# Kernel tuning notes

Measured on AMD Instinct MI355X. Metric: run time of the kernel, lower is better.

## Reference

```python
import jax, jax.numpy as jnp
import numpy as np

N_EMB = 512
N_HEADS = 8
HEAD_SIZE = N_EMB // N_HEADS  # 64
B, T = 4, 2048
EPS = 1e-5


def layernorm(x, g, b):
    mu = jnp.mean(x, axis=-1, keepdims=True)
    var = jnp.var(x, axis=-1, keepdims=True)
    return (x - mu) * jax.lax.rsqrt(var + EPS) * g + b


def setup_inputs() -> dict:
    key = jax.random.key(0)
    ks = jax.random.split(key, 8)
    s = 1.0 / np.sqrt(N_EMB)
    x = jax.random.normal(ks[0], (B, T, N_EMB), dtype=jnp.float32)
    # per-head q/k/v weights stacked: [H, n_emb, head_size]
    wq = jax.random.uniform(ks[1], (N_HEADS, N_EMB, HEAD_SIZE), minval=-s, maxval=s, dtype=jnp.float32)
    wk = jax.random.uniform(ks[2], (N_HEADS, N_EMB, HEAD_SIZE), minval=-s, maxval=s, dtype=jnp.float32)
    wv = jax.random.uniform(ks[3], (N_HEADS, N_EMB, HEAD_SIZE), minval=-s, maxval=s, dtype=jnp.float32)
    w_ff = jax.random.uniform(ks[4], (N_EMB, N_EMB), minval=-s, maxval=s, dtype=jnp.float32)
    b_ff = jax.random.uniform(ks[5], (N_EMB,), minval=-s, maxval=s, dtype=jnp.float32)
    ln1_g = jnp.ones((N_EMB,), jnp.float32)
    ln1_b = jnp.zeros((N_EMB,), jnp.float32)
    ln2_g = jnp.ones((N_EMB,), jnp.float32)
    ln2_b = jnp.zeros((N_EMB,), jnp.float32)
    return {"x": x, "wq": wq, "wk": wk, "wv": wv, "w_ff": w_ff, "b_ff": b_ff,
            "ln1_g": ln1_g, "ln1_b": ln1_b, "ln2_g": ln2_g, "ln2_b": ln2_b}


def reference(x, wq, wk, wv, w_ff, b_ff, ln1_g, ln1_b, ln2_g, ln2_b):
    # --- self-attention branch (dropout=0 -> identity) ---
    h = layernorm(x, ln1_g, ln1_b)                       # [B,T,C]
    q = jnp.einsum('btc,hcd->bhtd', h, wq)               # [B,H,T,d]
    k = jnp.einsum('btc,hcd->bhtd', h, wk)
    v = jnp.einsum('btc,hcd->bhtd', h, wv)
    scale = HEAD_SIZE ** -0.5
    wei = jnp.einsum('bhtd,bhsd->bhts', q, k) * scale    # [B,H,T,T]
    Tt = x.shape[1]
    causal = jnp.tril(jnp.ones((Tt, Tt), dtype=bool))
    wei = jnp.where(causal, wei, -jnp.inf)
    wei = jax.nn.softmax(wei, axis=-1)
    attn = jnp.einsum('bhts,bhsd->bhtd', wei, v)         # [B,H,T,d]
    # concat heads along last dim (head order preserved)
    Bn, H, Tn, d = attn.shape
    sa = jnp.transpose(attn, (0, 2, 1, 3)).reshape(Bn, Tn, H * d)
    x = x + sa
    # --- feed-forward branch: Linear + ReLU (dropout=0) ---
    h2 = layernorm(x, ln2_g, ln2_b)
    ff = jax.nn.relu(h2 @ w_ff + b_ff)
    return x + ff
```

## Files before the change

### kernel.cpp

```cpp
#include <hip/hip_runtime.h>

#define Bsz  4
#define Tseq 2048
#define Cdim 512
#define Hn   8
#define Dh   64
#define BT   8192
#define NQKV 1536
#define NEG_BIG (-1e30f)

typedef __attribute__((ext_vector_type(8))) short bf16x8;
typedef __attribute__((ext_vector_type(4))) short bf16x4;
typedef __attribute__((ext_vector_type(4))) float f32x4;

__device__ __forceinline__ float b2f(short s) {
    unsigned u = ((unsigned)(unsigned short)s) << 16;
    float f; __builtin_memcpy(&f, &u, 4); return f;
}
__device__ __forceinline__ short f2b(float f) {
    unsigned u; __builtin_memcpy(&u, &f, 4);
    u = (u + 0x7fffu + ((u >> 16) & 1u)) >> 16;
    return (short)u;
}
__device__ __forceinline__ void g2l16(const short* g, short* l) {
    __builtin_amdgcn_global_load_lds(
        (const __attribute__((address_space(1))) unsigned int*)(uintptr_t)g,
        (__attribute__((address_space(3))) unsigned int*)l, 16, 0, 0);
}

__global__ __launch_bounds__(256) void k_prep(const float* __restrict__ wq, const float* __restrict__ wk,
                                              const float* __restrict__ wv, const float* __restrict__ wff,
                                              short* __restrict__ wqkvt, short* __restrict__ wfft,
                                              const float* __restrict__ x, const float* __restrict__ g,
                                              const float* __restrict__ b, short* __restrict__ out) {
    const int blk = blockIdx.x, tid = threadIdx.x;
    if (blk < 256) {
        __shared__ float ldsT[64 * 65];
        if (blk < 192) {
            int hm = blk >> 3, ct = blk & 7;
            int proj = hm >> 3, h = hm & 7;
            const float* w = (proj == 0) ? wq : (proj == 1 ? wk : wv);
#pragma unroll
            for (int i = 0; i < 16; i++) {
                int flat = i * 256 + tid, cc = flat >> 6, dd = flat & 63;
                ldsT[dd * 65 + cc] = w[(h * 512 + ct * 64 + cc) * 64 + dd];
            }
            __syncthreads();
#pragma unroll
            for (int i = 0; i < 16; i++) {
                int flat = i * 256 + tid, dd = flat >> 6, cc = flat & 63;
                int n = proj * 512 + h * 64 + dd;
                wqkvt[n * 512 + ct * 64 + cc] = f2b(ldsT[dd * 65 + cc]);
            }
        } else {
            int b2 = blk - 192, rt = b2 >> 3, nt8 = b2 & 7;
#pragma unroll
            for (int i = 0; i < 16; i++) {
                int flat = i * 256 + tid, cc = flat >> 6, nn = flat & 63;
                ldsT[nn * 65 + cc] = wff[(rt * 64 + cc) * 512 + nt8 * 64 + nn];
            }
            __syncthreads();
#pragma unroll
            for (int i = 0; i < 16; i++) {
                int flat = i * 256 + tid, nn = flat >> 6, cc = flat & 63;
                wfft[(nt8 * 64 + nn) * 512 + rt * 64 + cc] = f2b(ldsT[nn * 65 + cc]);
            }
        }
    } else {
        int row  = (blk - 256) * 4 + (tid >> 6);
        int lane = tid & 63;
        const f32x4 a0 = *(const f32x4*)(x + row * Cdim + lane * 8);
        const f32x4 a1 = *(const f32x4*)(x + row * Cdim + lane * 8 + 4);
        float v[8] = {a0[0], a0[1], a0[2], a0[3], a1[0], a1[1], a1[2], a1[3]};
        float s = 0.f, sq = 0.f;
#pragma unroll
        for (int i = 0; i < 8; i++) { s += v[i]; sq += v[i] * v[i]; }
#pragma unroll
        for (int off = 1; off < 64; off <<= 1) { s += __shfl_xor(s, off); sq += __shfl_xor(sq, off); }
        float mean = s * (1.f / 512.f);
        float var  = sq * (1.f / 512.f) - mean * mean;
        float rstd = rsqrtf(var + 1e-5f);
        const f32x4 g0 = *(const f32x4*)(g + lane * 8);
        const f32x4 g1 = *(const f32x4*)(g + lane * 8 + 4);
        const f32x4 b0 = *(const f32x4*)(b + lane * 8);
        const f32x4 b1 = *(const f32x4*)(b + lane * 8 + 4);
        float gg[8] = {g0[0], g0[1], g0[2], g0[3], g1[0], g1[1], g1[2], g1[3]};
        float bb[8] = {b0[0], b0[1], b0[2], b0[3], b1[0], b1[1], b1[2], b1[3]};
        bf16x8 o;
#pragma unroll
        for (int i = 0; i < 8; i++) o[i] = f2b((v[i] - mean) * rstd * gg[i] + bb[i]);
        *(bf16x8*)(out + row * Cdim + lane * 8) = o;
    }
}

__global__ __launch_bounds__(256) void k_ln(const float* __restrict__ x, const float* __restrict__ g,
                                            const float* __restrict__ b, short* __restrict__ out) {
    int row  = blockIdx.x * 4 + (threadIdx.x >> 6);
    int lane = threadIdx.x & 63;
    const f32x4 a0 = *(const f32x4*)(x + row * Cdim + lane * 8);
    const f32x4 a1 = *(const f32x4*)(x + row * Cdim + lane * 8 + 4);
    float v[8] = {a0[0], a0[1], a0[2], a0[3], a1[0], a1[1], a1[2], a1[3]};
    float s = 0.f, sq = 0.f;
#pragma unroll
    for (int i = 0; i < 8; i++) { s += v[i]; sq += v[i] * v[i]; }
#pragma unroll
    for (int off = 1; off < 64; off <<= 1) { s += __shfl_xor(s, off); sq += __shfl_xor(sq, off); }
    float mean = s * (1.f / 512.f);
    float var  = sq * (1.f / 512.f) - mean * mean;
    float rstd = rsqrtf(var + 1e-5f);
    const f32x4 g0 = *(const f32x4*)(g + lane * 8);
    const f32x4 g1 = *(const f32x4*)(g + lane * 8 + 4);
    const f32x4 b0 = *(const f32x4*)(b + lane * 8);
    const f32x4 b1 = *(const f32x4*)(b + lane * 8 + 4);
    float gg[8] = {g0[0], g0[1], g0[2], g0[3], g1[0], g1[1], g1[2], g1[3]};
    float bb[8] = {b0[0], b0[1], b0[2], b0[3], b1[0], b1[1], b1[2], b1[3]};
    bf16x8 o;
#pragma unroll
    for (int i = 0; i < 8; i++) o[i] = f2b((v[i] - mean) * rstd * gg[i] + bb[i]);
    *(bf16x8*)(out + row * Cdim + lane * 8) = o;
}

__global__ __launch_bounds__(256) void k_gemm_qkv(const short* __restrict__ A, const short* __restrict__ Wt,
                                                  short* __restrict__ q, short* __restrict__ k,
                                                  short* __restrict__ vt) {
    const int tid = threadIdx.x;
    const int wave = tid >> 6, lane = tid & 63;
    const int quad = lane >> 4, l15 = lane & 15;
    const int m0 = blockIdx.x * 128, n0 = blockIdx.y * 128;
    const int wm = wave & 1, wn = wave >> 1;
    __shared__ __align__(16) short As[2][128 * 32];
    __shared__ __align__(16) short Bs[2][128 * 32];
    f32x4 acc[4][4];
#pragma unroll
    for (int i = 0; i < 4; i++)
#pragma unroll
        for (int j = 0; j < 4; j++) acc[i][j] = (f32x4){0.f, 0.f, 0.f, 0.f};
    const int lr = lane >> 2, lc = lane & 3;
    const short* Ag = A  + (m0 + wave * 32 + lr) * Cdim + lc * 8;
    const short* Bg = Wt + (n0 + wave * 32 + lr) * Cdim + lc * 8;
    g2l16(Ag,                  &As[0][wave * 1024]);
    g2l16(Ag + 16 * Cdim,      &As[0][wave * 1024 + 512]);
    g2l16(Bg,                  &Bs[0][wave * 1024]);
    g2l16(Bg + 16 * Cdim,      &Bs[0][wave * 1024 + 512]);
    g2l16(Ag + 32,             &As[1][wave * 1024]);
    g2l16(Ag + 16 * Cdim + 32, &As[1][wave * 1024 + 512]);
    g2l16(Bg + 32,             &Bs[1][wave * 1024]);
    g2l16(Bg + 16 * Cdim + 32, &Bs[1][wave * 1024 + 512]);
    for (int kk = 0; kk < 16; kk++) {
        const int cur = kk & 1;
        if (kk < 15) { asm volatile("s_waitcnt vmcnt(4)" ::: "memory"); }
        else         { asm volatile("s_waitcnt vmcnt(0)" ::: "memory"); }
        __builtin_amdgcn_s_barrier();
        __builtin_amdgcn_sched_barrier(0);
        bf16x8 a[4], w[4];
#pragma unroll
        for (int mt = 0; mt < 4; mt++) a[mt] = *(const bf16x8*)(&As[cur][(wm * 64 + mt * 16 + l15) * 32 + quad * 8]);
#pragma unroll
        for (int nt = 0; nt < 4; nt++) w[nt] = *(const bf16x8*)(&Bs[cur][(wn * 64 + nt * 16 + l15) * 32 + quad * 8]);
#pragma unroll
        for (int mt = 0; mt < 4; mt++)
#pragma unroll
            for (int nt = 0; nt < 4; nt++)
                acc[mt][nt] = __builtin_amdgcn_mfma_f32_16x16x32_bf16(a[mt], w[nt], acc[mt][nt], 0, 0, 0);
        __builtin_amdgcn_sched_barrier(0);
        __builtin_amdgcn_s_barrier();
        if (kk + 2 < 16) {
            const int k0 = (kk + 2) * 32;
            g2l16(Ag + k0,             &As[cur][wave * 1024]);
            g2l16(Ag + 16 * Cdim + k0, &As[cur][wave * 1024 + 512]);
            g2l16(Bg + k0,             &Bs[cur][wave * 1024]);
            g2l16(Bg + 16 * Cdim + k0, &Bs[cur][wave * 1024 + 512]);
        }
    }
    const int proj = n0 >> 9;
    const int n0w  = n0 + wn * 64;
    const int hh   = (n0w & 511) >> 6;
    const int m0w  = m0 + wm * 64;
#pragma unroll
    for (int mt = 0; mt < 4; mt++) {
#pragma unroll
        for (int r = 0; r < 4; r++) {
            int t  = m0w + mt * 16 + quad * 4 + r;
            int bi = t >> 11, tt = t & 2047;
#pragma unroll
            for (int nt = 0; nt < 4; nt++) {
                int d = nt * 16 + l15;
                short val = f2b(acc[mt][nt][r]);
                if (proj == 0)      q [((bi * Hn + hh) * Tseq + tt) * Dh + d] = val;
                else if (proj == 1) k [((bi * Hn + hh) * Tseq + tt) * Dh + d] = val;
                else                vt[((bi * Hn + hh) * Dh + d) * Tseq + tt] = val;
            }
        }
    }
}

__global__ __launch_bounds__(256, 3) void k_attn(const short* __restrict__ qb, const short* __restrict__ kb,
                                                 const short* __restrict__ vtb, const float* __restrict__ x,
                                                 float* __restrict__ out1) {
    const int wave = threadIdx.x >> 6, lane = threadIdx.x & 63;
    const int quad = lane >> 4, l15 = lane & 15;
    const int D  = blockIdx.y * 32 + blockIdx.x;
    const int j5 = D & 31;
    const int bh = (j5 & 7) * 4 + (j5 >> 3);
    const int u  = D >> 5, kq = u >> 3, d8 = u & 7;
    const int qg = (kq == 0) ? 31 - d8 : (kq == 1) ? 16 + d8 : (kq == 2) ? 15 - d8 : d8;
    const int q0  = qg * 64;
    const int qw0 = q0 + wave * 16;
    const int nkt = qg + 1;

    const short* Q = qb  + bh * Tseq * Dh;
    const short* K = kb  + bh * Tseq * Dh;
    const short* V = vtb + bh * Dh * Tseq;

    __shared__ __align__(16) short Ks[2][64 * 64];
    __shared__ __align__(16) short Vs[2][64 * 64];
    __shared__ __align__(16) short Ps[4][16 * 72];
    short* pw = &Ps[wave][0];

    const int lr8 = lane >> 3, lc8 = lane & 7;
    const int sw8 = (lc8 ^ lr8) << 3;
    const short* Ksrc = K + (wave * 16 + lr8) * Dh + sw8;
    const short* Vsrc = V + (wave * 16 + lr8) * Tseq + sw8;

    g2l16(Ksrc,            &Ks[0][wave * 1024]);
    g2l16(Ksrc + 8 * Dh,   &Ks[0][wave * 1024 + 512]);
    g2l16(Vsrc,            &Vs[0][wave * 1024]);
    g2l16(Vsrc + 8 * Tseq, &Vs[0][wave * 1024 + 512]);

    bf16x8 qa[2];
#pragma unroll
    for (int c = 0; c < 2; c++)
        qa[c] = *(const bf16x8*)(Q + (qw0 + l15) * Dh + c * 32 + quad * 8);

    f32x4 o[4];
#pragma unroll
    for (int i = 0; i < 4; i++) o[i] = (f32x4){0.f, 0.f, 0.f, 0.f};
    float m_i = NEG_BIG, l_i = 0.f;

    const float sc = 0.125f * 1.44269504089f;
    const int sx = l15 & 7;

    __syncthreads();

    for (int kt = 0; kt < nkt; kt++) {
        const short* Kb = &Ks[kt & 1][0];
        const short* Vb = &Vs[kt & 1][0];
        if (kt + 1 < nkt) {
            g2l16(Ksrc + (kt + 1) * 64 * Dh,            &Ks[(kt + 1) & 1][wave * 1024]);
            g2l16(Ksrc + (kt + 1) * 64 * Dh + 8 * Dh,   &Ks[(kt + 1) & 1][wave * 1024 + 512]);
            g2l16(Vsrc + (kt + 1) * 64,                 &Vs[(kt + 1) & 1][wave * 1024]);
            g2l16(Vsrc + (kt + 1) * 64 + 8 * Tseq,      &Vs[(kt + 1) & 1][wave * 1024 + 512]);
        }
        const int s0 = kt * 64;
        f32x4 st[4];
#pragma unroll
        for (int nt = 0; nt < 4; nt++) {
            bf16x8 k0 = *(const bf16x8*)(Kb + (nt * 16 + l15) * 64 + ((quad ^ sx) << 3));
            bf16x8 k1 = *(const bf16x8*)(Kb + (nt * 16 + l15) * 64 + (((4 | quad) ^ sx) << 3));
            f32x4 z = (f32x4){0.f, 0.f, 0.f, 0.f};
            z = __builtin_amdgcn_mfma_f32_16x16x32_bf16(k0, qa[0], z, 0, 0, 0);
            z = __builtin_amdgcn_mfma_f32_16x16x32_bf16(k1, qa[1], z, 0, 0, 0);
            st[nt] = z;
        }
        const int qq = qw0 + l15;
        if (kt == nkt - 1) {
#pragma unroll
            for (int nt = 0; nt < 4; nt++)
#pragma unroll
                for (int r = 0; r < 4; r++) {
                    int s = s0 + nt * 16 + quad * 4 + r;
                    st[nt][r] = (s > qq) ? NEG_BIG : st[nt][r] * sc;
                }
        } else {
#pragma unroll
            for (int nt = 0; nt < 4; nt++)
#pragma unroll
                for (int r = 0; r < 4; r++) st[nt][r] *= sc;
        }
        float mx = fmaxf(fmaxf(fmaxf(st[0][0], st[0][1]), fmaxf(st[0][2], st[0][3])),
                         fmaxf(fmaxf(st[1][0], st[1][1]), fmaxf(st[1][2], st[1][3])));
        mx = fmaxf(mx, fmaxf(fmaxf(fmaxf(st[2][0], st[2][1]), fmaxf(st[2][2], st[2][3])),
                             fmaxf(fmaxf(st[3][0], st[3][1]), fmaxf(st[3][2], st[3][3]))));
        mx = fmaxf(mx, __shfl_xor(mx, 16));
        mx = fmaxf(mx, __shfl_xor(mx, 32));
        float mn    = fmaxf(m_i, mx);
        float alpha = __builtin_amdgcn_exp2f(m_i - mn);
        m_i = mn;
        float rs = 0.f;
        bf16x4 pk[4];
#pragma unroll
        for (int nt = 0; nt < 4; nt++) {
#pragma unroll
            for (int r = 0; r < 4; r++) {
                float p = __builtin_amdgcn_exp2f(st[nt][r] - mn);
                rs += p;
                pk[nt][r] = f2b(p);
            }
        }
        rs += __shfl_xor(rs, 16);
        rs += __shfl_xor(rs, 32);
        l_i = l_i * alpha + rs;
#pragma unroll
        for (int nt = 0; nt < 4; nt++)
            *(bf16x4*)(pw + l15 * 72 + nt * 16 + quad * 4) = pk[nt];
#pragma unroll
        for (int r = 0; r < 4; r++) {
            float ar = __shfl(alpha, quad * 4 + r);
#pragma unroll
            for (int dt = 0; dt < 4; dt++) o[dt][r] *= ar;
        }
        asm volatile("s_waitcnt lgkmcnt(0)" ::: "memory");
        bf16x8 pa[2];
#pragma unroll
        for (int c = 0; c < 2; c++)
            pa[c] = *(const bf16x8*)(pw + l15 * 72 + c * 32 + quad * 8);
#pragma unroll
        for (int c = 0; c < 2; c++)
#pragma unroll
            for (int v4 = 0; v4 < 4; v4++) {
                bf16x8 vb = *(const bf16x8*)(Vb + (v4 * 16 + l15) * 64 + ((((c << 2) | quad) ^ sx) << 3));
                o[v4] = __builtin_amdgcn_mfma_f32_16x16x32_bf16(pa[c], vb, o[v4], 0, 0, 0);
            }
        __syncthreads();
    }
    const int bi = bh >> 3, hh = bh & 7;
#pragma unroll
    for (int r = 0; r < 4; r++) {
        int row = quad * 4 + r;
        float Lr  = __shfl(l_i, row);
        float inv = 1.f / Lr;
#pragma unroll
        for (int v4 = 0; v4 < 4; v4++) {
            int t   = qw0 + row;
            int idx = (bi * Tseq + t) * Cdim + hh * Dh + v4 * 16 + l15;
            out1[idx] = x[idx] + o[v4][r] * inv;
        }
    }
}

__global__ __launch_bounds__(256) void k_gemm_ff(const short* __restrict__ A, const short* __restrict__ Wt,
                                                 const float* __restrict__ bias, const float* __restrict__ res,
                                                 float* __restrict__ out) {
    const int tid = threadIdx.x;
    const int wave = tid >> 6, lane = tid & 63;
    const int quad = lane >> 4, l15 = lane & 15;
    const int m0 = blockIdx.x * 128, n0 = blockIdx.y * 64;
    const int wm = wave & 1, wn = wave >> 1;
    __shared__ __align__(16) short As[2][128 * 32];
    __shared__ __align__(16) short Bs[2][64 * 32];
    f32x4 acc[4][2];
#pragma unroll
    for (int i = 0; i < 4; i++)
#pragma unroll
        for (int j = 0; j < 2; j++) acc[i][j] = (f32x4){0.f, 0.f, 0.f, 0.f};
    const int lr = lane >> 2, lc = lane & 3;
    const short* Ag = A  + (m0 + wave * 32 + lr) * Cdim + lc * 8;
    const short* Bg = Wt + (n0 + wave * 16 + lr) * Cdim + lc * 8;
    g2l16(Ag,                  &As[0][wave * 1024]);
    g2l16(Ag + 16 * Cdim,      &As[0][wave * 1024 + 512]);
    g2l16(Bg,                  &Bs[0][wave * 512]);
    g2l16(Ag + 32,             &As[1][wave * 1024]);
    g2l16(Ag + 16 * Cdim + 32, &As[1][wave * 1024 + 512]);
    g2l16(Bg + 32,             &Bs[1][wave * 512]);
    for (int kk = 0; kk < 16; kk++) {
        const int cur = kk & 1;
        if (kk < 15) { asm volatile("s_waitcnt vmcnt(3)" ::: "memory"); }
        else         { asm volatile("s_waitcnt vmcnt(0)" ::: "memory"); }
        __builtin_amdgcn_s_barrier();
        __builtin_amdgcn_sched_barrier(0);
        bf16x8 a[4], w[2];
#pragma unroll
        for (int mt = 0; mt < 4; mt++) a[mt] = *(const bf16x8*)(&As[cur][(wm * 64 + mt * 16 + l15) * 32 + quad * 8]);
#pragma unroll
        for (int nt = 0; nt < 2; nt++) w[nt] = *(const bf16x8*)(&Bs[cur][(wn * 32 + nt * 16 + l15) * 32 + quad * 8]);
#pragma unroll
        for (int mt = 0; mt < 4; mt++)
#pragma unroll
            for (int nt = 0; nt < 2; nt++)
                acc[mt][nt] = __builtin_amdgcn_mfma_f32_16x16x32_bf16(a[mt], w[nt], acc[mt][nt], 0, 0, 0);
        __builtin_amdgcn_sched_barrier(0);
        __builtin_amdgcn_s_barrier();
        if (kk + 2 < 16) {
            const int k0 = (kk + 2) * 32;
            g2l16(Ag + k0,             &As[cur][wave * 1024]);
            g2l16(Ag + 16 * Cdim + k0, &As[cur][wave * 1024 + 512]);
            g2l16(Bg + k0,             &Bs[cur][wave * 512]);
        }
    }
    const int m0w = m0 + wm * 64, n0w = n0 + wn * 32;
#pragma unroll
    for (int mt = 0; mt < 4; mt++) {
#pragma unroll
        for (int r = 0; r < 4; r++) {
            int t = m0w + mt * 16 + quad * 4 + r;
#pragma unroll
            for (int nt = 0; nt < 2; nt++) {
                int n = n0w + nt * 16 + l15;
                float fv = acc[mt][nt][r] + bias[n];
                fv = fmaxf(fv, 0.f);
                out[t * Cdim + n] = res[t * Cdim + n] + fv;
            }
        }
    }
}

extern "C" void kernel_launch(void* const* d_in, const int* in_sizes, int n_in,
                              void* d_out, int out_size, void* d_ws, size_t ws_size,
                              hipStream_t stream) {
    const float* x   = (const float*)d_in[0];
    const float* wq  = (const float*)d_in[1];
    const float* wk  = (const float*)d_in[2];
    const float* wv  = (const float*)d_in[3];
    const float* wff = (const float*)d_in[4];
    const float* bff = (const float*)d_in[5];
    const float* g1  = (const float*)d_in[6];
    const float* b1  = (const float*)d_in[7];
    const float* g2  = (const float*)d_in[8];
    const float* b2  = (const float*)d_in[9];

    char* p = (char*)d_ws;
    short* wqkvt = (short*)p; p += (size_t)NQKV * Cdim * 2;
    short* wfft  = (short*)p; p += (size_t)Cdim * Cdim * 2;
    short* h1    = (short*)p; p += (size_t)BT * Cdim * 2;
    short* qb    = (short*)p; p += (size_t)BT * Cdim * 2;
    short* kb    = (short*)p; p += (size_t)BT * Cdim * 2;
    short* vtb   = (short*)p; p += (size_t)BT * Cdim * 2;
    float* out1  = (float*)p; p += (size_t)BT * Cdim * 4;

    hipLaunchKernelGGL(k_prep,     dim3(2304),    dim3(256), 0, stream,
                       wq, wk, wv, wff, wqkvt, wfft, x, g1, b1, h1);
    hipLaunchKernelGGL(k_gemm_qkv, dim3(64, 12),  dim3(256), 0, stream, h1, wqkvt, qb, kb, vtb);
    hipLaunchKernelGGL(k_attn,     dim3(32, 32),  dim3(256), 0, stream, qb, kb, vtb, x, out1);
    hipLaunchKernelGGL(k_ln,       dim3(2048),    dim3(256), 0, stream, out1, g2, b2, h1);
    hipLaunchKernelGGL(k_gemm_ff,  dim3(64, 8),   dim3(256), 0, stream, h1, wfft, bff, out1, (float*)d_out);
}
```

Measured before the change: 172.2 us.

## Stage V-transpose through LDS for coalesced stores; skip softmax rescale lazily

The QKV GEMM epilogue for the V projection now writes the accumulator tile transposed into shared memory, then stores contiguous 16-byte rows to the transposed V buffer. This replaces the scattered 2-byte global stores with coalesced ones, and the shared buffers are merged into one array so it can be reused for staging. In the attention kernel, the running-max update and the rescaling of the output accumulator are skipped unless the new max exceeds the old one by more than 8 (log2 units). This is a lazy-rescale trick that saves exp and multiply work per tile, at the cost of exponentials that can reach up to 2^8 before normalization.

```diff
diff --git a/kernel.cpp b/kernel.cpp
--- a/kernel.cpp
+++ b/kernel.cpp
@@ -128,8 +128,9 @@
     const int quad = lane >> 4, l15 = lane & 15;
     const int m0 = blockIdx.x * 128, n0 = blockIdx.y * 128;
     const int wm = wave & 1, wn = wave >> 1;
-    __shared__ __align__(16) short As[2][128 * 32];
-    __shared__ __align__(16) short Bs[2][128 * 32];
+    __shared__ __align__(16) short smem[17408];
+    short* As = smem;
+    short* Bs = smem + 8192;
     f32x4 acc[4][4];
 #pragma unroll
     for (int i = 0; i < 4; i++)
@@ -138,14 +139,14 @@
     const int lr = lane >> 2, lc = lane & 3;
     const short* Ag = A  + (m0 + wave * 32 + lr) * Cdim + lc * 8;
     const short* Bg = Wt + (n0 + wave * 32 + lr) * Cdim + lc * 8;
-    g2l16(Ag,                  &As[0][wave * 1024]);
-    g2l16(Ag + 16 * Cdim,      &As[0][wave * 1024 + 512]);
-    g2l16(Bg,                  &Bs[0][wave * 1024]);
-    g2l16(Bg + 16 * Cdim,      &Bs[0][wave * 1024 + 512]);
-    g2l16(Ag + 32,             &As[1][wave * 1024]);
-    g2l16(Ag + 16 * Cdim + 32, &As[1][wave * 1024 + 512]);
-    g2l16(Bg + 32,             &Bs[1][wave * 1024]);
-    g2l16(Bg + 16 * Cdim + 32, &Bs[1][wave * 1024 + 512]);
+    g2l16(Ag,                  As + wave * 1024);
+    g2l16(Ag + 16 * Cdim,      As + wave * 1024 + 512);
+    g2l16(Bg,                  Bs + wave * 1024);
+    g2l16(Bg + 16 * Cdim,      Bs + wave * 1024 + 512);
+    g2l16(Ag + 32,             As + 4096 + wave * 1024);
+    g2l16(Ag + 16 * Cdim + 32, As + 4096 + wave * 1024 + 512);
+    g2l16(Bg + 32,             Bs + 4096 + wave * 1024);
+    g2l16(Bg + 16 * Cdim + 32, Bs + 4096 + wave * 1024 + 512);
     for (int kk = 0; kk < 16; kk++) {
         const int cur = kk & 1;
         if (kk < 15) { asm volatile("s_waitcnt vmcnt(4)" ::: "memory"); }
@@ -154,9 +155,9 @@
         __builtin_amdgcn_sched_barrier(0);
         bf16x8 a[4], w[4];
 #pragma unroll
-        for (int mt = 0; mt < 4; mt++) a[mt] = *(const bf16x8*)(&As[cur][(wm * 64 + mt * 16 + l15) * 32 + quad * 8]);
-#pragma unroll
-        for (int nt = 0; nt < 4; nt++) w[nt] = *(const bf16x8*)(&Bs[cur][(wn * 64 + nt * 16 + l15) * 32 + quad * 8]);
+        for (int mt = 0; mt < 4; mt++) a[mt] = *(const bf16x8*)(As + cur * 4096 + (wm * 64 + mt * 16 + l15) * 32 + quad * 8);
+#pragma unroll
+        for (int nt = 0; nt < 4; nt++) w[nt] = *(const bf16x8*)(Bs + cur * 4096 + (wn * 64 + nt * 16 + l15) * 32 + quad * 8);
 #pragma unroll
         for (int mt = 0; mt < 4; mt++)
 #pragma unroll
@@ -166,30 +167,52 @@
         __builtin_amdgcn_s_barrier();
         if (kk + 2 < 16) {
             const int k0 = (kk + 2) * 32;
-            g2l16(Ag + k0,             &As[cur][wave * 1024]);
-            g2l16(Ag + 16 * Cdim + k0, &As[cur][wave * 1024 + 512]);
-            g2l16(Bg + k0,             &Bs[cur][wave * 1024]);
-            g2l16(Bg + 16 * Cdim + k0, &Bs[cur][wave * 1024 + 512]);
+            g2l16(Ag + k0,             As + cur * 4096 + wave * 1024);
+            g2l16(Ag + 16 * Cdim + k0, As + cur * 4096 + wave * 1024 + 512);
+            g2l16(Bg + k0,             Bs + cur * 4096 + wave * 1024);
+            g2l16(Bg + 16 * Cdim + k0, Bs + cur * 4096 + wave * 1024 + 512);
         }
     }
     const int proj = n0 >> 9;
     const int n0w  = n0 + wn * 64;
     const int hh   = (n0w & 511) >> 6;
     const int m0w  = m0 + wm * 64;
-#pragma unroll
-    for (int mt = 0; mt < 4; mt++) {
-#pragma unroll
-        for (int r = 0; r < 4; r++) {
-            int t  = m0w + mt * 16 + quad * 4 + r;
-            int bi = t >> 11, tt = t & 2047;
+    if (proj < 2) {
+#pragma unroll
+        for (int mt = 0; mt < 4; mt++) {
+#pragma unroll
+            for (int r = 0; r < 4; r++) {
+                int t  = m0w + mt * 16 + quad * 4 + r;
+                int bi = t >> 11, tt = t & 2047;
+#pragma unroll
+                for (int nt = 0; nt < 4; nt++) {
+                    int d = nt * 16 + l15;
+                    short val = f2b(acc[mt][nt][r]);
+                    if (proj == 0) q[((bi * Hn + hh) * Tseq + tt) * Dh + d] = val;
+                    else           k[((bi * Hn + hh) * Tseq + tt) * Dh + d] = val;
+                }
+            }
+        }
+    } else {
+        short* Tw = smem + wave * 4352;
+#pragma unroll
+        for (int mt = 0; mt < 4; mt++)
 #pragma unroll
             for (int nt = 0; nt < 4; nt++) {
-                int d = nt * 16 + l15;
-                short val = f2b(acc[mt][nt][r]);
-                if (proj == 0)      q [((bi * Hn + hh) * Tseq + tt) * Dh + d] = val;
-                else if (proj == 1) k [((bi * Hn + hh) * Tseq + tt) * Dh + d] = val;
-                else                vt[((bi * Hn + hh) * Dh + d) * Tseq + tt] = val;
-            }
+                bf16x4 pk;
+#pragma unroll
+                for (int r = 0; r < 4; r++) pk[r] = f2b(acc[mt][nt][r]);
+                *(bf16x4*)(Tw + (nt * 16 + l15) * 68 + mt * 16 + quad * 4) = pk;
+            }
+        asm volatile("s_waitcnt lgkmcnt(0)" ::: "memory");
+        const int bi = m0 >> 11, tt0 = m0w & 2047;
+        const int g8 = lane >> 3, h8 = lane & 7;
+        short* vbase = vt + ((size_t)(bi * Hn + hh) * Dh) * Tseq;
+#pragma unroll
+        for (int p = 0; p < 8; p++) {
+            int dl = p * 8 + g8;
+            bf16x8 row = *(const bf16x8*)(Tw + dl * 68 + h8 * 8);
+            *(bf16x8*)(vbase + (size_t)dl * Tseq + tt0 + h8 * 8) = row;
         }
     }
 }
@@ -283,32 +306,35 @@
                              fmaxf(fmaxf(st[3][0], st[3][1]), fmaxf(st[3][2], st[3][3]))));
         mx = fmaxf(mx, __shfl_xor(mx, 16));
         mx = fmaxf(mx, __shfl_xor(mx, 32));
-        float mn    = fmaxf(m_i, mx);
-        float alpha = __builtin_amdgcn_exp2f(m_i - mn);
-        m_i = mn;
+        if (!__all(mx <= m_i + 8.f)) {
+            float mn    = fmaxf(m_i, mx);
+            float alpha = __builtin_amdgcn_exp2f(m_i - mn);
+            m_i = mn;
+            l_i *= alpha;
+#pragma unroll
+            for (int r = 0; r < 4; r++) {
+                float ar = __shfl(alpha, quad * 4 + r);
+#pragma unroll
+                for (int dt = 0; dt < 4; dt++) o[dt][r] *= ar;
+            }
+        }
         float rs = 0.f;
         bf16x4 pk[4];
 #pragma unroll
         for (int nt = 0; nt < 4; nt++) {
 #pragma unroll
             for (int r = 0; r < 4; r++) {
-                float p = __builtin_amdgcn_exp2f(st[nt][r] - mn);
+                float p = __builtin_amdgcn_exp2f(st[nt][r] - m_i);
                 rs += p;
                 pk[nt][r] = f2b(p);
             }
         }
         rs += __shfl_xor(rs, 16);
         rs += __shfl_xor(rs, 32);
-        l_i = l_i * alpha + rs;
+        l_i += rs;
 #pragma unroll
         for (int nt = 0; nt < 4; nt++)
             *(bf16x4*)(pw + l15 * 72 + nt * 16 + quad * 4) = pk[nt];
-#pragma unroll
-        for (int r = 0; r < 4; r++) {
-            float ar = __shfl(alpha, quad * 4 + r);
-#pragma unroll
-            for (int dt = 0; dt < 4; dt++) o[dt][r] *= ar;
-        }
         asm volatile("s_waitcnt lgkmcnt(0)" ::: "memory");
         bf16x8 pa[2];
 #pragma unroll
```

After: 165.8 us. 1.04x faster.
